# Kernel tuning notes

Measured on AMD Instinct MI355X. Metric: run time of the kernel, lower is better.

## Reference

```python
import jax, jax.numpy as jnp
import numpy as np
from jax import lax


def _causal_mask(shape, mask_center):
    # shape = (out_ch, in_ch, h, w); mirrors CausalConv2d mask construction
    o, i, h, w = shape
    m = np.zeros(shape, dtype=np.float32)
    m[:, :, : h // 2, :] = 1.0
    m[:, :, h // 2, : w // 2 + (0 if mask_center else 1)] = 1.0
    return jnp.asarray(m)

MASK1 = _causal_mask((16, 1, 7, 7), mask_center=True)
MASK2 = _causal_mask((16, 16, 3, 3), mask_center=False)


def _conv(x, w, b, pad):
    y = lax.conv_general_dilated(
        x, w, window_strides=(1, 1), padding=[(pad, pad), (pad, pad)],
        dimension_numbers=("NCHW", "OIHW", "NCHW"))
    return y + b[None, :, None, None]


def setup_inputs() -> dict:
    key = jax.random.key(0)
    ks = jax.random.split(key, 7)
    B, H, W = 1024, 64, 64
    x = jax.random.uniform(ks[0], (B, 1, H, W), dtype=jnp.float32)
    # Kaiming-ish init scales
    w1 = jax.random.normal(ks[1], (16, 1, 7, 7), jnp.float32) * (1.0 / np.sqrt(1 * 49))
    b1 = jax.random.normal(ks[2], (16,), jnp.float32) * 0.01
    w2 = jax.random.normal(ks[3], (16, 16, 3, 3), jnp.float32) * (1.0 / np.sqrt(16 * 9))
    b2 = jax.random.normal(ks[4], (16,), jnp.float32) * 0.01
    w3 = jax.random.normal(ks[5], (1, 16, 1, 1), jnp.float32) * (1.0 / np.sqrt(16))
    b3 = jax.random.normal(ks[6], (1,), jnp.float32) * 0.01
    return {"x": x, "w1": w1, "b1": b1, "w2": w2, "b2": b2, "w3": w3, "b3": b3}


def reference(x, w1, b1, w2, b2, w3, b3):
    # PixelCNN._forward: masked conv7x7 -> relu -> masked conv3x3 -> relu -> conv1x1 -> sigmoid
    h = jax.nn.relu(_conv(x, w1 * MASK1, b1, pad=3))
    h = jax.nn.relu(_conv(h, w2 * MASK2, b2, pad=1))
    return jax.nn.sigmoid(_conv(h, w3, b3, pad=0))
```

## Files before the change

### kernel.cpp

```cpp
#include <hip/hip_runtime.h>

typedef _Float16 half8  __attribute__((ext_vector_type(8)));
typedef __fp16   fp16x2 __attribute__((ext_vector_type(2)));
typedef float    floatx4 __attribute__((ext_vector_type(4)));
typedef float    f4a __attribute__((ext_vector_type(4), aligned(4)));

#define IMG_H 64
#define IMG_W 64
#define TH 16
#define INW 72
#define H1W 66
#define H1H 17
#define PLDW (H1H*H1W*2)
#define CP 1440
#define CPM1 1439
#define S16N (4*CP + 4)

__device__ __forceinline__ unsigned pk2u(float a, float b) {
    fp16x2 h = __builtin_amdgcn_cvt_pkrtz(a, b);
    return __builtin_bit_cast(unsigned, h);
}

__global__ __launch_bounds__(512, 8) void pixelcnn_mfma12(
    const float* __restrict__ x,
    const float* __restrict__ w1, const float* __restrict__ b1,
    const float* __restrict__ w2, const float* __restrict__ b2,
    const float* __restrict__ w3, const float* __restrict__ b3,
    float* __restrict__ out)
{
    __shared__ __align__(16) _Float16      s16[S16N];
    __shared__ __align__(16) unsigned char s_w2t8[16 * 96];
    __shared__ __align__(16) unsigned      s_h1[2 * PLDW];

    const int t    = threadIdx.x;
    const int lane = t & 63;
    const int wave = t >> 6;
    const int n    = lane & 15;
    const int quad = lane >> 4;
    const int s    = wave >> 2;
    const int x0q  = wave & 3;
    const int img  = blockIdx.y;
    const int ty0  = blockIdx.x * TH;

    const float* xim = x + img * (IMG_H * IMG_W);

    const float* wr = w1 + n * 49 + quad * 7;
    f4a wlo = *(const f4a*)wr;
    f4a whi = *(const f4a*)(wr + 3);
    const floatx4 bias1 = *(const floatx4*)(b1 + quad * 4);
    const floatx4 bias2 = *(const floatx4*)(b2 + quad * 4);
    const floatx4 w3q   = *(const floatx4*)(w3 + quad * 4);
    const float   bias3 = b3[0];
    half8 af;
    {
        bool q3 = (quad == 3);
        af[0] = (_Float16)wlo[0];
        af[1] = (_Float16)wlo[1];
        af[2] = (_Float16)wlo[2];
        af[3] = (_Float16)(q3 ? 0.f : wlo[3]);
        af[4] = (_Float16)(q3 ? 0.f : whi[1]);
        af[5] = (_Float16)(q3 ? 0.f : whi[2]);
        af[6] = (_Float16)(q3 ? 0.f : whi[3]);
        af[7] = (_Float16)0.f;
    }

    if (t < 360) {
        int r = t / 18, c4 = (t - r * 18) * 4;
        int gy = ty0 - 4 + r;
        int gx0 = c4 - 4;
        float4 v  = {0.f, 0.f, 0.f, 0.f};
        float4 v2 = {0.f, 0.f, 0.f, 0.f};
        if ((unsigned)gy < IMG_H) {
            const float* rp = xim + gy * IMG_W;
            if ((unsigned)gx0 < IMG_W)       v  = *(const float4*)(rp + gx0);
            if ((unsigned)(gx0 + 4) < IMG_W) v2 = *(const float4*)(rp + gx0 + 4);
        }
        unsigned a0 = pk2u(v.x,  v.y),  a1 = pk2u(v.z,  v.w);
        unsigned a2 = pk2u(v2.x, v2.y), a3 = pk2u(v2.z, v2.w);
        unsigned m10 = (a0 >> 16) | (a1 << 16);
        unsigned m21 = (a1 >> 16) | (a2 << 16);
        unsigned m32 = (a2 >> 16) | (a3 << 16);
        int lin = r * INW + c4;
        *(uint2*)&s16[0*CP + 4 + lin] = uint2{a0,  a1 };
        *(uint2*)&s16[1*CP + 4 + lin] = uint2{m10, m21};
        *(uint2*)&s16[2*CP + 4 + lin] = uint2{a1,  a2 };
        *(uint2*)&s16[3*CP + 4 + lin] = uint2{m21, m32};
    } else if (t < 394) {
        int idx = t - 360;
        int cell = (idx >> 1) * H1W + ((idx & 1) ? 65 : 0);
        *(uint2*)&s_h1[cell * 2]        = uint2{0u, 0u};
        *(uint2*)&s_h1[PLDW + cell * 2] = uint2{0u, 0u};
    }
    if (t >= 256) {
        int ch = (t >> 4) & 15, l = t & 15;
        const float* w2cl = w2 + (ch * 16 + l) * 9;
#pragma unroll
        for (int j = 0; j < 6; ++j) {
            float v = (j < 5) ? w2cl[j] : 0.f;
            unsigned q8 = (unsigned)__builtin_amdgcn_cvt_pk_fp8_f32(v, 0.f, 0, false);
            s_w2t8[ch * 96 + j * 16 + l] = (unsigned char)(q8 & 0xff);
        }
    }
    __syncthreads();

    {
        const int px = x0q * 16 + n;
        const int S  = px + 1;
        const int c  = S & 3;
        const _Float16* ap0 = &s16[c * CPM1 + 4 + S + (s * 8 + quad) * INW];
        const unsigned wd0 = (unsigned)((quad >> 1) * PLDW + ((s * 8) * H1W + S) * 2 + (quad & 1));
        const bool top = (ty0 == 0) && (s == 0);

#pragma unroll
        for (int i = 0; i < 9; ++i) {
            if (i == 0 && s != 0) continue;
            const _Float16* ap = ap0 + i * INW;
            uint2 lo = *(const uint2*)ap;
            uint2 hi = *(const uint2*)(ap + 4);
            uint4 bu; bu.x = lo.x; bu.y = lo.y; bu.z = hi.x; bu.w = hi.y;
            half8 b = __builtin_bit_cast(half8, bu);
            floatx4 acc = bias1;
            acc = __builtin_amdgcn_mfma_f32_16x16x32_f16(af, b, acc, 0, 0, 0);
            int d = __builtin_amdgcn_cvt_pk_fp8_f32(fmaxf(acc[0], 0.f), fmaxf(acc[1], 0.f), 0, false);
            d = __builtin_amdgcn_cvt_pk_fp8_f32(fmaxf(acc[2], 0.f), fmaxf(acc[3], 0.f), d, true);
            unsigned dv = (unsigned)d;
            if (i == 0 && top) dv = 0u;
            s_h1[wd0 + i * (H1W * 2)] = dv;
        }
    }
    __syncthreads();

    {
        const long w2f0 = *(const long*)&s_w2t8[n * 96 +  0 + quad * 8];
        const long w2f1 = *(const long*)&s_w2t8[n * 96 + 32 + quad * 8];
        const long w2f2 = *(const long*)&s_w2t8[n * 96 + 64 + quad * 8];
        const int x0 = x0q * 16;
        const int tqh = quad >> 1, plane = quad & 1;
        const int E0 = (s * 8 + 1) * H1W + x0 + n + 1;
        const char* h1b = (const char*)s_h1 + plane * (PLDW * 4);
        const char* a0 = h1b + (E0 - H1W - 1 + tqh) * 8;
        const char* a1 = h1b + (E0 + (tqh ? -1 : -(H1W - 1))) * 8;
        const char* a2 = h1b + E0 * 8;
        float* sbase = out + ((img * IMG_H) + ty0 + s * 8 + quad) * IMG_W + x0 + n;

#pragma unroll
        for (int g = 0; g < 2; ++g) {
            float sv0, sv1, sv2, sv3;
#pragma unroll
            for (int q = 0; q < 4; ++q) {
                const int k = g * 4 + q;
                floatx4 acc = bias2;
                acc = __builtin_amdgcn_mfma_f32_16x16x32_fp8_fp8(w2f0, *(const long*)(a0 + k * 528), acc, 0, 0, 0);
                acc = __builtin_amdgcn_mfma_f32_16x16x32_fp8_fp8(w2f1, *(const long*)(a1 + k * 528), acc, 0, 0, 0);
                acc = __builtin_amdgcn_mfma_f32_16x16x32_fp8_fp8(w2f2, *(const long*)(a2 + k * 528), acc, 0, 0, 0);
                float sacc = fmaxf(acc[0], 0.f) * w3q[0];
                sacc = fmaf(fmaxf(acc[1], 0.f), w3q[1], sacc);
                sacc = fmaf(fmaxf(acc[2], 0.f), w3q[2], sacc);
                sacc = fmaf(fmaxf(acc[3], 0.f), w3q[3], sacc);
                sacc += __shfl_xor(sacc, 16);
                sacc += __shfl_xor(sacc, 32);
                if      (q == 0) sv0 = sacc;
                else if (q == 1) sv1 = sacc;
                else if (q == 2) sv2 = sacc;
                else             sv3 = sacc;
            }
            float t01 = (quad & 1) ? sv1 : sv0;
            float t23 = (quad & 1) ? sv3 : sv2;
            float v   = (quad & 2) ? t23 : t01;
            float r = __builtin_amdgcn_rcpf(1.f + __expf(-(v + bias3)));
            *(float*)((char*)sbase + g * 1024) = r;
        }
    }
}

extern "C" void kernel_launch(void* const* d_in, const int* in_sizes, int n_in,
                              void* d_out, int out_size, void* d_ws, size_t ws_size,
                              hipStream_t stream) {
    const float* x  = (const float*)d_in[0];
    const float* w1 = (const float*)d_in[1];
    const float* b1 = (const float*)d_in[2];
    const float* w2 = (const float*)d_in[3];
    const float* b2 = (const float*)d_in[4];
    const float* w3 = (const float*)d_in[5];
    const float* b3 = (const float*)d_in[6];
    float* out = (float*)d_out;

    dim3 grid(4, 1024);
    dim3 block(512);
    hipLaunchKernelGGL(pixelcnn_mfma12, grid, block, 0, stream,
                       x, w1, b1, w2, b2, w3, b3, out);
}
```

Measured before the change: 101.2 us.

## Process two images per block and overlap next input staging with conv2

Each block now handles two images, so the grid's y dimension is halved. The fp8 w2 weight transform and the address setup are done once per block instead of once per image. The second image's input is loaded into shared memory while the first image's conv2/1x1 stage runs, which overlaps global loads with MFMA work. In exchange there are fewer blocks to spread across the GPU, an extra barrier per image, and possibly more register pressure. Correctness depends on phase2 reading only s_h1 while stage writes only s16.

```diff
diff --git a/kernel.cpp b/kernel.cpp
--- a/kernel.cpp
+++ b/kernel.cpp
@@ -21,7 +21,7 @@
     return __builtin_bit_cast(unsigned, h);
 }
 
-__global__ __launch_bounds__(512, 8) void pixelcnn_mfma12(
+__global__ __launch_bounds__(512, 8) void pixelcnn_mfma14(
     const float* __restrict__ x,
     const float* __restrict__ w1, const float* __restrict__ b1,
     const float* __restrict__ w2, const float* __restrict__ b2,
@@ -39,10 +39,12 @@
     const int quad = lane >> 4;
     const int s    = wave >> 2;
     const int x0q  = wave & 3;
-    const int img  = blockIdx.y;
     const int ty0  = blockIdx.x * TH;
-
-    const float* xim = x + img * (IMG_H * IMG_W);
+    const int img0 = blockIdx.y * 2;
+
+    const float* xim0 = x + img0 * (IMG_H * IMG_W);
+    const float* xim1 = xim0 + IMG_H * IMG_W;
+    float* outb = out + img0 * (IMG_H * IMG_W);
 
     const float* wr = w1 + n * 49 + quad * 7;
     f4a wlo = *(const f4a*)wr;
@@ -64,53 +66,44 @@
         af[7] = (_Float16)0.f;
     }
 
-    if (t < 360) {
-        int r = t / 18, c4 = (t - r * 18) * 4;
-        int gy = ty0 - 4 + r;
-        int gx0 = c4 - 4;
-        float4 v  = {0.f, 0.f, 0.f, 0.f};
-        float4 v2 = {0.f, 0.f, 0.f, 0.f};
-        if ((unsigned)gy < IMG_H) {
-            const float* rp = xim + gy * IMG_W;
-            if ((unsigned)gx0 < IMG_W)       v  = *(const float4*)(rp + gx0);
-            if ((unsigned)(gx0 + 4) < IMG_W) v2 = *(const float4*)(rp + gx0 + 4);
-        }
-        unsigned a0 = pk2u(v.x,  v.y),  a1 = pk2u(v.z,  v.w);
-        unsigned a2 = pk2u(v2.x, v2.y), a3 = pk2u(v2.z, v2.w);
-        unsigned m10 = (a0 >> 16) | (a1 << 16);
-        unsigned m21 = (a1 >> 16) | (a2 << 16);
-        unsigned m32 = (a2 >> 16) | (a3 << 16);
-        int lin = r * INW + c4;
-        *(uint2*)&s16[0*CP + 4 + lin] = uint2{a0,  a1 };
-        *(uint2*)&s16[1*CP + 4 + lin] = uint2{m10, m21};
-        *(uint2*)&s16[2*CP + 4 + lin] = uint2{a1,  a2 };
-        *(uint2*)&s16[3*CP + 4 + lin] = uint2{m21, m32};
-    } else if (t < 394) {
-        int idx = t - 360;
-        int cell = (idx >> 1) * H1W + ((idx & 1) ? 65 : 0);
-        *(uint2*)&s_h1[cell * 2]        = uint2{0u, 0u};
-        *(uint2*)&s_h1[PLDW + cell * 2] = uint2{0u, 0u};
-    }
-    if (t >= 256) {
-        int ch = (t >> 4) & 15, l = t & 15;
-        const float* w2cl = w2 + (ch * 16 + l) * 9;
-#pragma unroll
-        for (int j = 0; j < 6; ++j) {
-            float v = (j < 5) ? w2cl[j] : 0.f;
-            unsigned q8 = (unsigned)__builtin_amdgcn_cvt_pk_fp8_f32(v, 0.f, 0, false);
-            s_w2t8[ch * 96 + j * 16 + l] = (unsigned char)(q8 & 0xff);
-        }
-    }
-    __syncthreads();
-
-    {
-        const int px = x0q * 16 + n;
-        const int S  = px + 1;
-        const int c  = S & 3;
-        const _Float16* ap0 = &s16[c * CPM1 + 4 + S + (s * 8 + quad) * INW];
-        const unsigned wd0 = (unsigned)((quad >> 1) * PLDW + ((s * 8) * H1W + S) * 2 + (quad & 1));
-        const bool top = (ty0 == 0) && (s == 0);
-
+    const int px_ = x0q * 16 + n;
+    const int S_  = px_ + 1;
+    const _Float16* ap0 = &s16[(S_ & 3) * CPM1 + 4 + S_ + (s * 8 + quad) * INW];
+    const unsigned wd0 = (unsigned)((quad >> 1) * PLDW + ((s * 8) * H1W + S_) * 2 + (quad & 1));
+    const bool top = (ty0 == 0) && (s == 0);
+    const int tqh = quad >> 1, plane = quad & 1;
+    const int E0 = (s * 8 + 1) * H1W + x0q * 16 + n + 1;
+    const char* h1b = (const char*)s_h1 + plane * (PLDW * 4);
+    const char* a0 = h1b + (E0 - H1W - 1 + tqh) * 8;
+    const char* a1 = h1b + (E0 + (tqh ? -1 : -(H1W - 1))) * 8;
+    const char* a2 = h1b + E0 * 8;
+
+    auto stage = [&](const float* xim) {
+        if (t < 360) {
+            int r = t / 18, c4 = (t - r * 18) * 4;
+            int gy = ty0 - 4 + r;
+            int gx0 = c4 - 4;
+            float4 v  = {0.f, 0.f, 0.f, 0.f};
+            float4 v2 = {0.f, 0.f, 0.f, 0.f};
+            if ((unsigned)gy < IMG_H) {
+                const float* rp = xim + gy * IMG_W;
+                if ((unsigned)gx0 < IMG_W)       v  = *(const float4*)(rp + gx0);
+                if ((unsigned)(gx0 + 4) < IMG_W) v2 = *(const float4*)(rp + gx0 + 4);
+            }
+            unsigned a0w = pk2u(v.x,  v.y),  a1w = pk2u(v.z,  v.w);
+            unsigned a2w = pk2u(v2.x, v2.y), a3w = pk2u(v2.z, v2.w);
+            unsigned m10 = (a0w >> 16) | (a1w << 16);
+            unsigned m21 = (a1w >> 16) | (a2w << 16);
+            unsigned m32 = (a2w >> 16) | (a3w << 16);
+            int lin = r * INW + c4;
+            *(uint2*)&s16[0*CP + 4 + lin] = uint2{a0w, a1w};
+            *(uint2*)&s16[1*CP + 4 + lin] = uint2{m10, m21};
+            *(uint2*)&s16[2*CP + 4 + lin] = uint2{a1w, a2w};
+            *(uint2*)&s16[3*CP + 4 + lin] = uint2{m21, m32};
+        }
+    };
+
+    auto phase1 = [&]() {
 #pragma unroll
         for (int i = 0; i < 9; ++i) {
             if (i == 0 && s != 0) continue;
@@ -127,22 +120,33 @@
             if (i == 0 && top) dv = 0u;
             s_h1[wd0 + i * (H1W * 2)] = dv;
         }
+    };
+
+    stage(xim0);
+    if (t >= 360 && t < 394) {
+        int idx = t - 360;
+        int cell = (idx >> 1) * H1W + ((idx & 1) ? 65 : 0);
+        *(uint2*)&s_h1[cell * 2]        = uint2{0u, 0u};
+        *(uint2*)&s_h1[PLDW + cell * 2] = uint2{0u, 0u};
     }
-    __syncthreads();
-
-    {
-        const long w2f0 = *(const long*)&s_w2t8[n * 96 +  0 + quad * 8];
-        const long w2f1 = *(const long*)&s_w2t8[n * 96 + 32 + quad * 8];
-        const long w2f2 = *(const long*)&s_w2t8[n * 96 + 64 + quad * 8];
-        const int x0 = x0q * 16;
-        const int tqh = quad >> 1, plane = quad & 1;
-        const int E0 = (s * 8 + 1) * H1W + x0 + n + 1;
-        const char* h1b = (const char*)s_h1 + plane * (PLDW * 4);
-        const char* a0 = h1b + (E0 - H1W - 1 + tqh) * 8;
-        const char* a1 = h1b + (E0 + (tqh ? -1 : -(H1W - 1))) * 8;
-        const char* a2 = h1b + E0 * 8;
-        float* sbase = out + ((img * IMG_H) + ty0 + s * 8 + quad) * IMG_W + x0 + n;
-
+    if (t >= 256) {
+        int ch = (t >> 4) & 15, l = t & 15;
+        const float* w2cl = w2 + (ch * 16 + l) * 9;
+#pragma unroll
+        for (int j = 0; j < 6; ++j) {
+            float v = (j < 5) ? w2cl[j] : 0.f;
+            unsigned q8 = (unsigned)__builtin_amdgcn_cvt_pk_fp8_f32(v, 0.f, 0, false);
+            s_w2t8[ch * 96 + j * 16 + l] = (unsigned char)(q8 & 0xff);
+        }
+    }
+    __syncthreads();
+
+    const long w2f0 = *(const long*)&s_w2t8[n * 96 +  0 + quad * 8];
+    const long w2f1 = *(const long*)&s_w2t8[n * 96 + 32 + quad * 8];
+    const long w2f2 = *(const long*)&s_w2t8[n * 96 + 64 + quad * 8];
+
+    auto phase2 = [&](float* outim) {
+        float* sbase = outim + (ty0 + s * 8 + quad) * IMG_W + x0q * 16 + n;
 #pragma unroll
         for (int g = 0; g < 2; ++g) {
             float sv0, sv1, sv2, sv3;
@@ -170,7 +174,16 @@
             float r = __builtin_amdgcn_rcpf(1.f + __expf(-(v + bias3)));
             *(float*)((char*)sbase + g * 1024) = r;
         }
-    }
+    };
+
+    phase1();
+    __syncthreads();
+    stage(xim1);
+    phase2(outb);
+    __syncthreads();
+    phase1();
+    __syncthreads();
+    phase2(outb + IMG_H * IMG_W);
 }
 
 extern "C" void kernel_launch(void* const* d_in, const int* in_sizes, int n_in,
@@ -185,8 +198,8 @@
     const float* b3 = (const float*)d_in[6];
     float* out = (float*)d_out;
 
-    dim3 grid(4, 1024);
+    dim3 grid(4, 512);
     dim3 block(512);
-    hipLaunchKernelGGL(pixelcnn_mfma12, grid, block, 0, stream,
+    hipLaunchKernelGGL(pixelcnn_mfma14, grid, block, 0, stream,
                        x, w1, b1, w2, b2, w3, b3, out);
 }
```

Result: no change. 102.1 us (+0.8%).
